# Kernel tuning notes

Measured on AMD Instinct MI355X. Metric: run time of the kernel, lower is better.

## Reference

```python
import jax, jax.numpy as jnp
import numpy as np

NH = 32          # nh * 2 neighbors per point (init nh=16)
P_REDUCTION = 0.5


def setup_inputs() -> dict:
    key = jax.random.key(0)
    k1, k2 = jax.random.split(key)
    x = jax.random.normal(k1, (2, 8192, 256), dtype=jnp.float32)       # [b, n, e]
    coords = jax.random.normal(k2, (2, 2, 8192, 1), dtype=jnp.float32) # [b, c, n, 1]
    return {"x": x, "coords": coords}


def _knn_gather(x, coords):
    """Return features of the NH nearest neighbors of each point: [b, n, NH, e]."""
    cs = coords[..., 0]                                   # [b, c, n]
    sq = jnp.sum(cs * cs, axis=1)                         # [b, n]
    # squared euclidean distances [b, n, n]
    d2 = sq[:, :, None] + sq[:, None, :] - 2.0 * jnp.einsum('bcn,bcm->bnm', cs, cs)
    d2 = jax.lax.stop_gradient(d2)                        # indices are non-differentiable
    _, nn_idx = jax.lax.top_k(-d2, NH)                    # [b, n, NH] nearest points
    # gather neighbor features: [b, 1, n, e] indexed with [b, n, NH, 1] -> [b, n, NH, e]
    x_nh = jnp.take_along_axis(x[:, None, :, :], nn_idx[..., None], axis=2)
    return x_nh


def _forward(x, coords):
    b, n, e = x.shape
    x_nh = _knn_gather(x, coords)                         # [b, n, NH, e]
    # unbiased std over the neighbor dim (torch.std default, ddof=1)
    mean_nh = jnp.mean(x_nh, axis=-2, keepdims=True)
    local_s = jnp.sqrt(jnp.sum((x_nh - mean_nh) ** 2, axis=-2) / (NH - 1))  # [b, n, e]
    global_m = jnp.abs(jnp.mean(x, axis=1))               # [b, e]
    local_dist = jnp.sum(local_s / global_m[:, None, :], axis=-1)           # [b, n]
    n_keep = int((1.0 - P_REDUCTION) * n)
    _, keep_idx = jax.lax.top_k(local_dist, n_keep)       # [b, n_keep], sorted desc
    x_out = jnp.take_along_axis(x, keep_idx[:, :, None], axis=1)            # [b, n_keep, e]
    coords_out = jnp.take_along_axis(coords, keep_idx[:, None, :, None], axis=2)  # [b, c, n_keep, 1]
    return x_out, coords_out, local_dist


def reference(x, coords):
    return _forward(x, coords)
```

## Files before the change

kernel.cpp:

```cpp
#include <hip/hip_runtime.h>

#define NN 8192
#define EE 256
#define KNH 32
#define NKEEP 4096
#define NCX 64
#define NCELL 4096
#define CNT_MIN 48

typedef unsigned long long u64;
typedef unsigned int u32;


__device__ __forceinline__ int cellof(float v) {
    const int q = (int)floorf((v + 4.6f) * (64.0f / 9.2f));
    return min(max(q, 0), NCX - 1);
}

__global__ void __launch_bounds__(1024) k_pre(const float* __restrict__ coords,
                                              const float* __restrict__ x,
                                              int* __restrict__ start,
                                              float2* __restrict__ sc,
                                              int* __restrict__ sj,
                                              float* __restrict__ part) {
    __shared__ int cnt[NCELL];
    __shared__ int wsum[16];
    const int blk = blockIdx.x;
    if (blk >= 2) {
        float* fred = (float*)cnt;
        const int unit  = blk - 2;
        const int b     = unit >> 5;
        const int chunk = unit & 31;
        const int col   = threadIdx.x & 255;
        const int qtr   = threadIdx.x >> 8;
        const float* xp = x + ((size_t)b * NN + (size_t)chunk * 256 + (size_t)qtr * 64) * EE + col;
        float s = 0.0f;
        for (int r = 0; r < 64; ++r) s += xp[(size_t)r * EE];
        fred[threadIdx.x] = s;
        __syncthreads();
        if (threadIdx.x < 256) {
            const float tot = fred[threadIdx.x] + fred[threadIdx.x + 256]
                            + fred[threadIdx.x + 512] + fred[threadIdx.x + 768];
            part[((size_t)b * 32 + chunk) * EE + threadIdx.x] = tot;
        }
        return;
    }
    const int b = blk, t = threadIdx.x;
    const int lane = t & 63, wv = t >> 6;
#pragma unroll
    for (int k = 0; k < 4; ++k) cnt[k * 1024 + t] = 0;
    __syncthreads();
#pragma unroll
    for (int k = 0; k < 8; ++k) {
        const int i = k * 1024 + t;
        const float xv = coords[(size_t)b * 2 * NN + i];
        const float yv = coords[(size_t)b * 2 * NN + NN + i];
        atomicAdd(&cnt[cellof(xv) * NCX + cellof(yv)], 1);
    }
    __syncthreads();
    const int v0 = cnt[t * 4 + 0], v1 = cnt[t * 4 + 1];
    const int v2 = cnt[t * 4 + 2], v3 = cnt[t * 4 + 3];
    const int s = v0 + v1 + v2 + v3;
    int inc = s;
#pragma unroll
    for (int d = 1; d < 64; d <<= 1) {
        const int u = __shfl_up(inc, d);
        inc += (lane >= d) ? u : 0;
    }
    if (lane == 63) wsum[wv] = inc;
    __syncthreads();
    int wpre = 0;
#pragma unroll
    for (int w = 0; w < 16; ++w) wpre += (w < wv) ? wsum[w] : 0;
    int run = wpre + inc - s;
    start[b * (NCELL + 1) + t * 4 + 0] = run; cnt[t * 4 + 0] = run; run += v0;
    start[b * (NCELL + 1) + t * 4 + 1] = run; cnt[t * 4 + 1] = run; run += v1;
    start[b * (NCELL + 1) + t * 4 + 2] = run; cnt[t * 4 + 2] = run; run += v2;
    start[b * (NCELL + 1) + t * 4 + 3] = run; cnt[t * 4 + 3] = run; run += v3;
    if (t == 0) start[b * (NCELL + 1) + NCELL] = NN;
    __syncthreads();
#pragma unroll
    for (int k = 0; k < 8; ++k) {
        const int i = k * 1024 + t;
        const float xv = coords[(size_t)b * 2 * NN + i];
        const float yv = coords[(size_t)b * 2 * NN + NN + i];
        const int p = atomicAdd(&cnt[cellof(xv) * NCX + cellof(yv)], 1);
        sc[(size_t)b * NN + p] = make_float2(xv, yv);
        sj[(size_t)b * NN + p] = i;
    }
}

__global__ void k_gm_final(const float* __restrict__ part, float* __restrict__ gm) {
    const int b = blockIdx.y, t = threadIdx.x;
    float s = 0.0f;
    for (int c = 0; c < 32; ++c) s += part[((size_t)b * 32 + c) * EE + t];
    gm[b * EE + t] = fabsf(s / (float)NN);
}

__device__ __forceinline__ u64 shfl_xor_u64(u64 v, int m) {
    const u32 hi = (u32)__shfl_xor((int)(u32)(v >> 32), m);
    const u32 lo = (u32)__shfl_xor((int)(u32)v, m);
    return ((u64)hi << 32) | lo;
}

__device__ __forceinline__ u64 wave_min_u64(u64 h) {
#pragma unroll
    for (int s = 1; s < 64; s <<= 1) {
        const u64 o = shfl_xor_u64(h, s);
        h = (o < h) ? o : h;
    }
    return h;
}

__global__ void __launch_bounds__(256) k_knn_dist(
        const float* __restrict__ x,
        const float* __restrict__ gm, const float2* __restrict__ sc,
        const int* __restrict__ sj, const int* __restrict__ start,
        float* __restrict__ ld_out) {
    __shared__ u64 comp[4][64];
    const int wg   = blockIdx.x;
    const int swz  = (wg & 7) * 512 + (wg >> 3);
    const int b    = swz >> 11;
    const int pb   = swz & 2047;
    const int wid  = threadIdx.x >> 6;
    const int lane = threadIdx.x & 63;
    const int p    = pb * 4 + wid;

    const float2* scb = sc + (size_t)b * NN;
    const int*    sjb = sj + (size_t)b * NN;
    const int*    stb = start + b * (NCELL + 1);
    const float2 cp = scb[p];
    const int    i  = sjb[p];
    const float ci0 = cp.x, ci1 = cp.y;
    const int qx = cellof(ci0), qy = cellof(ci1);

    int xl, yl, yh, nsl;
    int myc0 = 0, mylen = 0;
    {
        const int xl0 = max(qx - 1, 0), xh0 = min(qx + 1, NCX - 1);
        const int yl0 = max(qy - 1, 0), yh0 = min(qy + 1, NCX - 1);
        const int ns0 = xh0 - xl0 + 1;
        int a0 = 0, a1 = 0;
        if (lane < ns0) { a0 = stb[(xl0 + lane) * NCX + yl0]; a1 = stb[(xl0 + lane) * NCX + yh0 + 1]; }
        const int xl1 = max(qx - 2, 0), xh1 = min(qx + 2, NCX - 1);
        const int yl1 = max(qy - 2, 0), yh1 = min(qy + 2, NCX - 1);
        const int ns1 = xh1 - xl1 + 1;
        int b0 = 0, b1 = 0;
        if (lane < ns1) { b0 = stb[(xl1 + lane) * NCX + yl1]; b1 = stb[(xl1 + lane) * NCX + yh1 + 1]; }
        const int xl2 = max(qx - 4, 0), xh2c = min(qx + 4, NCX - 1);
        const int yl2 = max(qy - 4, 0), yh2c = min(qy + 4, NCX - 1);
        const int ns2 = xh2c - xl2 + 1;
        int e0 = 0, e1 = 0;
        if (lane < ns2) { e0 = stb[(xl2 + lane) * NCX + yl2]; e1 = stb[(xl2 + lane) * NCX + yh2c + 1]; }

        const int l0 = a1 - a0, l1 = b1 - b0, l2 = e1 - e0;
        int t0 = l0, t1 = l1, t2 = l2;
#pragma unroll
        for (int s = 1; s < 64; s <<= 1) {
            t0 += __shfl_xor(t0, s);
            t1 += __shfl_xor(t1, s);
            t2 += __shfl_xor(t2, s);
        }
        if (t0 >= CNT_MIN) {
            xl = xl0; yl = yl0; yh = yh0; nsl = ns0; myc0 = a0; mylen = l0;
        } else if (t1 >= CNT_MIN) {
            xl = xl1; yl = yl1; yh = yh1; nsl = ns1; myc0 = b0; mylen = l1;
        } else if (t2 >= CNT_MIN) {
            xl = xl2; yl = yl2; yh = yh2c; nsl = ns2; myc0 = e0; mylen = l2;
        } else {
            int r = 8;
            for (;;) {
                xl = max(qx - r, 0);
                const int xh = min(qx + r, NCX - 1);
                yl = max(qy - r, 0);
                yh = min(qy + r, NCX - 1);
                nsl = xh - xl + 1;
                int c0 = 0, c1 = 0;
                if (lane < nsl) {
                    c0 = stb[(xl + lane) * NCX + yl];
                    c1 = stb[(xl + lane) * NCX + yh + 1];
                }
                myc0 = c0; mylen = c1 - c0;
                int tot = mylen;
#pragma unroll
                for (int s = 1; s < 64; s <<= 1) tot += __shfl_xor(tot, s);
                if (tot >= CNT_MIN || r >= NCX) break;
                r <<= 1;
            }
        }
    }
    int incl = mylen;
#pragma unroll
    for (int d = 1; d < 64; d <<= 1) {
        const int v = __shfl_up(incl, d);
        incl += (lane >= d) ? v : 0;
    }
    int excl = incl - mylen;
    const int L1 = __shfl(incl, 63);

    float dmin = 1e30f;
    for (int g = 0; g < L1; g += 128) {
        const int gp0 = g + lane;
        const int gp1 = g + 64 + lane;
        int lo0 = 0, hi0 = nsl - 1, lo1 = 0, hi1 = nsl - 1;
#pragma unroll
        for (int st = 0; st < 6; ++st) {
            const int mid0 = (lo0 + hi0 + 1) >> 1;
            const int mid1 = (lo1 + hi1 + 1) >> 1;
            const int v0 = __shfl(excl, mid0);
            const int v1 = __shfl(excl, mid1);
            const bool go0 = (v0 <= gp0), go1 = (v1 <= gp1);
            lo0 = go0 ? mid0 : lo0; hi0 = go0 ? hi0 : mid0 - 1;
            lo1 = go1 ? mid1 : lo1; hi1 = go1 ? hi1 : mid1 - 1;
        }
        const int cnd0 = __shfl(myc0, lo0) + gp0 - __shfl(excl, lo0);
        const int cnd1 = __shfl(myc0, lo1) + gp1 - __shfl(excl, lo1);
        const int cc0 = min(max(cnd0, 0), NN - 1);
        const int cc1 = min(max(cnd1, 0), NN - 1);
        const float2 pt0 = scb[cc0];
        const float2 pt1 = scb[cc1];
        const float dx0 = ci0 - pt0.x, dy0 = ci1 - pt0.y;
        const float dx1 = ci0 - pt1.x, dy1 = ci1 - pt1.y;
        const float d0 = fmaf(dx0, dx0, dy0 * dy0);
        const float d1 = fmaf(dx1, dx1, dy1 * dy1);
        if (gp0 < L1) dmin = fminf(dmin, d0);
        if (gp1 < L1) dmin = fminf(dmin, d1);
    }

    u32 mk = __float_as_uint(dmin);
#pragma unroll
    for (int k = 2; k <= 64; k <<= 1) {
#pragma unroll
        for (int j = k >> 1; j > 0; j >>= 1) {
            const u32 o = (u32)__shfl_xor((int)mk, j);
            const bool keep_min = (((lane & j) == 0) == ((lane & k) == 0));
            const u32 mn = min(mk, o), mx = max(mk, o);
            mk = keep_min ? mn : mx;
        }
    }
    const u32 T = (u32)__shfl((int)mk, 31);

    const float srad = sqrtf(__uint_as_float(T)) * 1.0002f + 1e-5f;
    xl = cellof(ci0 - srad);
    const int xh2 = cellof(ci0 + srad);
    yl = cellof(ci1 - srad);
    yh = cellof(ci1 + srad);
    nsl = xh2 - xl + 1;
    {
        int c0 = 0, c1 = 0;
        if (lane < nsl) {
            c0 = stb[(xl + lane) * NCX + yl];
            c1 = stb[(xl + lane) * NCX + yh + 1];
        }
        myc0 = c0; mylen = c1 - c0;
    }
    incl = mylen;
#pragma unroll
    for (int d = 1; d < 64; d <<= 1) {
        const int v = __shfl_up(incl, d);
        incl += (lane >= d) ? v : 0;
    }
    excl = incl - mylen;
    const int L2 = __shfl(incl, 63);

    const u64 lmask = (1ull << lane) - 1;
    int base = 0;
    for (int g = 0; g < L2; g += 128) {
        const int gp0 = g + lane;
        const int gp1 = g + 64 + lane;
        int lo0 = 0, hi0 = nsl - 1, lo1 = 0, hi1 = nsl - 1;
#pragma unroll
        for (int st = 0; st < 6; ++st) {
            const int mid0 = (lo0 + hi0 + 1) >> 1;
            const int mid1 = (lo1 + hi1 + 1) >> 1;
            const int v0 = __shfl(excl, mid0);
            const int v1 = __shfl(excl, mid1);
            const bool go0 = (v0 <= gp0), go1 = (v1 <= gp1);
            lo0 = go0 ? mid0 : lo0; hi0 = go0 ? hi0 : mid0 - 1;
            lo1 = go1 ? mid1 : lo1; hi1 = go1 ? hi1 : mid1 - 1;
        }
        const int cnd0 = __shfl(myc0, lo0) + gp0 - __shfl(excl, lo0);
        const int cnd1 = __shfl(myc0, lo1) + gp1 - __shfl(excl, lo1);
        const int cc0 = min(max(cnd0, 0), NN - 1);
        const int cc1 = min(max(cnd1, 0), NN - 1);
        const float2 pt0 = scb[cc0];
        const float2 pt1 = scb[cc1];
        const int jj0 = sjb[cc0];
        const int jj1 = sjb[cc1];
        const float dx0 = ci0 - pt0.x, dy0 = ci1 - pt0.y;
        const float dx1 = ci0 - pt1.x, dy1 = ci1 - pt1.y;
        const u32 db0 = __float_as_uint(fmaf(dx0, dx0, dy0 * dy0));
        const u32 db1 = __float_as_uint(fmaf(dx1, dx1, dy1 * dy1));
        const bool k0 = (gp0 < L2) && (db0 <= T);
        const bool k1 = (gp1 < L2) && (db1 <= T);
        const u64 m0 = __ballot(k0);
        const int pos0 = base + __popcll(m0 & lmask);
        base += __popcll(m0);
        if (k0 && pos0 < 64) comp[wid][pos0] = ((u64)db0 << 32) | (u32)jj0;
        const u64 m1 = __ballot(k1);
        const int pos1 = base + __popcll(m1 & lmask);
        base += __popcll(m1);
        if (k1 && pos1 < 64) comp[wid][pos1] = ((u64)db1 << 32) | (u32)jj1;
    }
    const bool ovf = (base > 64) || (base < KNH);

    u64 key = (lane < base) ? comp[wid][lane] : ~0ull;
#pragma unroll
    for (int k = 2; k <= 64; k <<= 1) {
#pragma unroll
        for (int j = k >> 1; j > 0; j >>= 1) {
            const u64 other = shfl_xor_u64(key, j);
            const bool keep_min = (((lane & j) == 0) == ((lane & k) == 0));
            const bool lt = (key < other);
            const u64 mn = lt ? key : other;
            const u64 mx = lt ? other : key;
            key = keep_min ? mn : mx;
        }
    }
    int jkeep = (int)(u32)key;

    if (ovf) {
        u64 minkeep = 0;
        for (int k = 0; k < KNH; ++k) {
            u64 best = ~0ull;
            for (int g = 0; g < L2; g += 64) {
                const int gp = g + lane;
                int lo = 0, hi = nsl - 1;
#pragma unroll
                for (int st = 0; st < 6; ++st) {
                    const int mid = (lo + hi + 1) >> 1;
                    const int v = __shfl(excl, mid);
                    const bool go = (v <= gp);
                    lo = go ? mid : lo;
                    hi = go ? hi : mid - 1;
                }
                const int cnd = __shfl(myc0, lo) + gp - __shfl(excl, lo);
                const int cc  = min(max(cnd, 0), NN - 1);
                const float2 pt = scb[cc];
                const int    jj = sjb[cc];
                const float dx = ci0 - pt.x, dy = ci1 - pt.y;
                const float d  = fmaf(dx, dx, dy * dy);
                const u64 kk = ((u64)__float_as_uint(d) << 32) | (u32)jj;
                if (gp < L2 && kk >= minkeep && kk < best) best = kk;
            }
            const u64 h = wave_min_u64(best);
            if (lane == k) jkeep = (int)(u32)h;
            minkeep = h + 1;
        }
    }

    float s1[4] = {0.f, 0.f, 0.f, 0.f};
    float s2[4] = {0.f, 0.f, 0.f, 0.f};
    const float* xb = x + (size_t)b * NN * EE;
#pragma unroll 8
    for (int k = 0; k < KNH; ++k) {
        const int j = __builtin_amdgcn_readlane(jkeep, k);
        const float4 v = *reinterpret_cast<const float4*>(xb + (size_t)j * EE + (lane << 2));
        s1[0] += v.x; s2[0] += v.x * v.x;
        s1[1] += v.y; s2[1] += v.y * v.y;
        s1[2] += v.z; s2[2] += v.z * v.z;
        s1[3] += v.w; s2[3] += v.w * v.w;
    }

    const float* gmb = gm + b * EE;
    float tt = 0.f;
#pragma unroll
    for (int q = 0; q < 4; ++q) {
        const float sum = s1[q];
        float ssd = s2[q] - sum * sum * (1.0f / 32.0f);
        ssd = ssd > 0.f ? ssd : 0.f;
        const float ls = sqrtf(ssd * (1.0f / 31.0f));
        tt += ls / gmb[(lane << 2) + q];
    }
#pragma unroll
    for (int s2r = 1; s2r < 64; s2r <<= 1) tt += __shfl_xor(tt, s2r);

    if (lane == 0) ld_out[(size_t)b * NN + i] = tt;
}

__global__ void k_rank_gather(const float* __restrict__ x, const float* __restrict__ coords,
                              const float* __restrict__ ld,
                              float* __restrict__ x_out, float* __restrict__ c_out) {
    const int b    = blockIdx.y;
    const int wid  = threadIdx.x >> 6;
    const int lane = threadIdx.x & 63;
    const int i    = blockIdx.x * 4 + wid;
    const float* lb = ld + (size_t)b * NN;
    const float di = lb[i];
    int cnt = 0;
    for (int t = 0; t < NN / 256; ++t) {
        const int j0 = t * 256 + (lane << 2);
        const float4 dv = *reinterpret_cast<const float4*>(lb + j0);
        cnt += (dv.x > di || (dv.x == di && (j0 + 0) < i)) ? 1 : 0;
        cnt += (dv.y > di || (dv.y == di && (j0 + 1) < i)) ? 1 : 0;
        cnt += (dv.z > di || (dv.z == di && (j0 + 2) < i)) ? 1 : 0;
        cnt += (dv.w > di || (dv.w == di && (j0 + 3) < i)) ? 1 : 0;
    }
#pragma unroll
    for (int s = 1; s < 64; s <<= 1) cnt += __shfl_xor(cnt, s);

    if (cnt < NKEEP) {
        const float4 v = *reinterpret_cast<const float4*>(x + ((size_t)b * NN + i) * EE + (lane << 2));
        *reinterpret_cast<float4*>(x_out + ((size_t)b * NKEEP + cnt) * EE + (lane << 2)) = v;
        if (lane < 2) {
            c_out[((size_t)b * 2 + lane) * NKEEP + cnt] = coords[((size_t)b * 2 + lane) * NN + i];
        }
    }
}

extern "C" void kernel_launch(void* const* d_in, const int* in_sizes, int n_in,
                              void* d_out, int out_size, void* d_ws, size_t ws_size,
                              hipStream_t stream) {
    const float* x      = (const float*)d_in[0];
    const float* coords = (const float*)d_in[1];

    float* out    = (float*)d_out;
    float* x_out  = out;
    float* c_out  = out + 2097152;
    float* ld_out = out + 2113536;

    char*   ws    = (char*)d_ws;
    float*  part  = (float*)(ws);
    float*  gm    = (float*)(ws + 65536);
    int*    start = (int*)  (ws + 67584);
    float2* sc    = (float2*)(ws + 100384);
    int*    sj    = (int*)  (ws + 231456);

    k_pre        <<<66,            1024, 0, stream>>>(coords, x, start, sc, sj, part);
    k_gm_final   <<<dim3(1, 2),    256,  0, stream>>>(part, gm);
    k_knn_dist   <<<4096,          256,  0, stream>>>(x, gm, sc, sj, start, ld_out);
    k_rank_gather<<<dim3(2048, 2), 256,  0, stream>>>(x, coords, ld_out, x_out, c_out);
}
```

Baseline: 83.85 us.

## Reuse first-pass candidate distances in registers when refine box is contained

The first KNN pass now keeps the first 256 candidate distances and indices in registers. When the refined search box fits inside the first box and that box held at most 256 candidates, the second pass compacts from those registers instead of re-reading the cell table and recomputing distances. The rare exact fallback is moved into a noinline function to reduce register pressure and code size in the main path. This adds live registers during the first pass, which could lower occupancy.

```diff
diff --git a/kernel.cpp b/kernel.cpp
--- a/kernel.cpp
+++ b/kernel.cpp
@@ -112,6 +112,52 @@
     return h;
 }
 
+__device__ __noinline__ int exact_fb(const float2* scb, const int* sjb, const int* stb,
+                                     float cx, float cy, int xl, int xh, int yl, int yh,
+                                     int lane) {
+    const int nsl = xh - xl + 1;
+    int c0 = 0, c1 = 0;
+    if (lane < nsl) { c0 = stb[(xl + lane) * NCX + yl]; c1 = stb[(xl + lane) * NCX + yh + 1]; }
+    const int myc = c0, len = c1 - c0;
+    int inc = len;
+#pragma unroll
+    for (int d = 1; d < 64; d <<= 1) {
+        const int v = __shfl_up(inc, d);
+        inc += (lane >= d) ? v : 0;
+    }
+    const int ex = inc - len;
+    const int L = __shfl(inc, 63);
+    int jk = 0;
+    u64 minkeep = 0;
+    for (int k = 0; k < KNH; ++k) {
+        u64 best = ~0ull;
+        for (int g = 0; g < L; g += 64) {
+            const int gp = g + lane;
+            int lo = 0, hi = nsl - 1;
+#pragma unroll
+            for (int st = 0; st < 6; ++st) {
+                const int mid = (lo + hi + 1) >> 1;
+                const int v = __shfl(ex, mid);
+                const bool go = (v <= gp);
+                lo = go ? mid : lo;
+                hi = go ? hi : mid - 1;
+            }
+            const int cnd = __shfl(myc, lo) + gp - __shfl(ex, lo);
+            const int cc = min(max(cnd, 0), NN - 1);
+            const float2 pt = scb[cc];
+            const int jj = sjb[cc];
+            const float dx = cx - pt.x, dy = cy - pt.y;
+            const float d = fmaf(dx, dx, dy * dy);
+            const u64 kk = ((u64)__float_as_uint(d) << 32) | (u32)jj;
+            if (gp < L && kk >= minkeep && kk < best) best = kk;
+        }
+        const u64 h = wave_min_u64(best);
+        if (lane == k) jk = (int)(u32)h;
+        minkeep = h + 1;
+    }
+    return jk;
+}
+
 __global__ void __launch_bounds__(256) k_knn_dist(
         const float* __restrict__ x,
         const float* __restrict__ gm, const float2* __restrict__ sc,
@@ -189,6 +235,7 @@
             }
         }
     }
+    const int xh1box = xl + nsl - 1;
     int incl = mylen;
 #pragma unroll
     for (int d = 1; d < 64; d <<= 1) {
@@ -199,7 +246,43 @@
     const int L1 = __shfl(incl, 63);
 
     float dmin = 1e30f;
-    for (int g = 0; g < L1; g += 128) {
+    u32 kdb0 = 0xFFFFFFFFu, kdb1 = 0xFFFFFFFFu, kdb2 = 0xFFFFFFFFu, kdb3 = 0xFFFFFFFFu;
+    int  kjj0 = 0, kjj1 = 0, kjj2 = 0, kjj3 = 0;
+
+#define CHUNK2(G, DB0, JJ0, DB1, JJ1)                                       \
+    do {                                                                    \
+        const int gp0 = (G) + lane;                                         \
+        const int gp1 = (G) + 64 + lane;                                    \
+        int lo0 = 0, hi0 = nsl - 1, lo1 = 0, hi1 = nsl - 1;                 \
+        _Pragma("unroll")                                                   \
+        for (int st = 0; st < 6; ++st) {                                    \
+            const int mid0 = (lo0 + hi0 + 1) >> 1;                          \
+            const int mid1 = (lo1 + hi1 + 1) >> 1;                          \
+            const int v0 = __shfl(excl, mid0);                              \
+            const int v1 = __shfl(excl, mid1);                              \
+            const bool go0 = (v0 <= gp0), go1 = (v1 <= gp1);                \
+            lo0 = go0 ? mid0 : lo0; hi0 = go0 ? hi0 : mid0 - 1;             \
+            lo1 = go1 ? mid1 : lo1; hi1 = go1 ? hi1 : mid1 - 1;             \
+        }                                                                   \
+        const int cnd0 = __shfl(myc0, lo0) + gp0 - __shfl(excl, lo0);       \
+        const int cnd1 = __shfl(myc0, lo1) + gp1 - __shfl(excl, lo1);       \
+        const int cc0 = min(max(cnd0, 0), NN - 1);                          \
+        const int cc1 = min(max(cnd1, 0), NN - 1);                          \
+        const float2 pt0 = scb[cc0];                                        \
+        const float2 pt1 = scb[cc1];                                        \
+        const int j0_ = sjb[cc0];                                           \
+        const int j1_ = sjb[cc1];                                           \
+        const float dx0 = ci0 - pt0.x, dy0 = ci1 - pt0.y;                   \
+        const float dx1 = ci0 - pt1.x, dy1 = ci1 - pt1.y;                   \
+        const float d0 = fmaf(dx0, dx0, dy0 * dy0);                         \
+        const float d1 = fmaf(dx1, dx1, dy1 * dy1);                         \
+        if (gp0 < L1) { dmin = fminf(dmin, d0); DB0 = __float_as_uint(d0); JJ0 = j0_; } \
+        if (gp1 < L1) { dmin = fminf(dmin, d1); DB1 = __float_as_uint(d1); JJ1 = j1_; } \
+    } while (0)
+
+    CHUNK2(0, kdb0, kjj0, kdb1, kjj1);
+    if (L1 > 128) CHUNK2(128, kdb2, kjj2, kdb3, kjj3);
+    for (int g = 256; g < L1; g += 128) {
         const int gp0 = g + lane;
         const int gp1 = g + 64 + lane;
         int lo0 = 0, hi0 = nsl - 1, lo1 = 0, hi1 = nsl - 1;
@@ -241,66 +324,68 @@
     const u32 T = (u32)__shfl((int)mk, 31);
 
     const float srad = sqrtf(__uint_as_float(T)) * 1.0002f + 1e-5f;
-    xl = cellof(ci0 - srad);
-    const int xh2 = cellof(ci0 + srad);
-    yl = cellof(ci1 - srad);
-    yh = cellof(ci1 + srad);
-    nsl = xh2 - xl + 1;
-    {
-        int c0 = 0, c1 = 0;
-        if (lane < nsl) {
-            c0 = stb[(xl + lane) * NCX + yl];
-            c1 = stb[(xl + lane) * NCX + yh + 1];
-        }
-        myc0 = c0; mylen = c1 - c0;
-    }
-    incl = mylen;
-#pragma unroll
-    for (int d = 1; d < 64; d <<= 1) {
-        const int v = __shfl_up(incl, d);
-        incl += (lane >= d) ? v : 0;
-    }
-    excl = incl - mylen;
-    const int L2 = __shfl(incl, 63);
+    const int p2xl = cellof(ci0 - srad), p2xh = cellof(ci0 + srad);
+    const int p2yl = cellof(ci1 - srad), p2yh = cellof(ci1 + srad);
+    const bool contained = (L1 <= 256) && (p2xl >= xl) && (p2xh <= xh1box) &&
+                           (p2yl >= yl) && (p2yh <= yh);
 
     const u64 lmask = (1ull << lane) - 1;
     int base = 0;
-    for (int g = 0; g < L2; g += 128) {
-        const int gp0 = g + lane;
-        const int gp1 = g + 64 + lane;
-        int lo0 = 0, hi0 = nsl - 1, lo1 = 0, hi1 = nsl - 1;
-#pragma unroll
-        for (int st = 0; st < 6; ++st) {
-            const int mid0 = (lo0 + hi0 + 1) >> 1;
-            const int mid1 = (lo1 + hi1 + 1) >> 1;
-            const int v0 = __shfl(excl, mid0);
-            const int v1 = __shfl(excl, mid1);
-            const bool go0 = (v0 <= gp0), go1 = (v1 <= gp1);
-            lo0 = go0 ? mid0 : lo0; hi0 = go0 ? hi0 : mid0 - 1;
-            lo1 = go1 ? mid1 : lo1; hi1 = go1 ? hi1 : mid1 - 1;
-        }
-        const int cnd0 = __shfl(myc0, lo0) + gp0 - __shfl(excl, lo0);
-        const int cnd1 = __shfl(myc0, lo1) + gp1 - __shfl(excl, lo1);
-        const int cc0 = min(max(cnd0, 0), NN - 1);
-        const int cc1 = min(max(cnd1, 0), NN - 1);
-        const float2 pt0 = scb[cc0];
-        const float2 pt1 = scb[cc1];
-        const int jj0 = sjb[cc0];
-        const int jj1 = sjb[cc1];
-        const float dx0 = ci0 - pt0.x, dy0 = ci1 - pt0.y;
-        const float dx1 = ci0 - pt1.x, dy1 = ci1 - pt1.y;
-        const u32 db0 = __float_as_uint(fmaf(dx0, dx0, dy0 * dy0));
-        const u32 db1 = __float_as_uint(fmaf(dx1, dx1, dy1 * dy1));
-        const bool k0 = (gp0 < L2) && (db0 <= T);
-        const bool k1 = (gp1 < L2) && (db1 <= T);
-        const u64 m0 = __ballot(k0);
-        const int pos0 = base + __popcll(m0 & lmask);
-        base += __popcll(m0);
-        if (k0 && pos0 < 64) comp[wid][pos0] = ((u64)db0 << 32) | (u32)jj0;
-        const u64 m1 = __ballot(k1);
-        const int pos1 = base + __popcll(m1 & lmask);
-        base += __popcll(m1);
-        if (k1 && pos1 < 64) comp[wid][pos1] = ((u64)db1 << 32) | (u32)jj1;
+
+#define COMPACT(DB, JJ)                                                     \
+    do {                                                                    \
+        const bool keep = ((DB) <= T);                                      \
+        const u64 m = __ballot(keep);                                       \
+        const int pos = base + __popcll(m & lmask);                         \
+        base += __popcll(m);                                                \
+        if (keep && pos < 64) comp[wid][pos] = ((u64)(DB) << 32) | (u32)(JJ); \
+    } while (0)
+
+    if (contained) {
+        COMPACT(kdb0, kjj0);
+        COMPACT(kdb1, kjj1);
+        COMPACT(kdb2, kjj2);
+        COMPACT(kdb3, kjj3);
+    } else {
+        const int nsl2 = p2xh - p2xl + 1;
+        int c0 = 0, c1 = 0;
+        if (lane < nsl2) {
+            c0 = stb[(p2xl + lane) * NCX + p2yl];
+            c1 = stb[(p2xl + lane) * NCX + p2yh + 1];
+        }
+        const int myc2 = c0;
+        const int len2 = c1 - c0;
+        int incl2 = len2;
+#pragma unroll
+        for (int d = 1; d < 64; d <<= 1) {
+            const int v = __shfl_up(incl2, d);
+            incl2 += (lane >= d) ? v : 0;
+        }
+        const int excl2 = incl2 - len2;
+        const int L2 = __shfl(incl2, 63);
+        for (int g = 0; g < L2; g += 64) {
+            const int gp = g + lane;
+            int lo = 0, hi = nsl2 - 1;
+#pragma unroll
+            for (int st = 0; st < 6; ++st) {
+                const int mid = (lo + hi + 1) >> 1;
+                const int v = __shfl(excl2, mid);
+                const bool go = (v <= gp);
+                lo = go ? mid : lo;
+                hi = go ? hi : mid - 1;
+            }
+            const int cnd = __shfl(myc2, lo) + gp - __shfl(excl2, lo);
+            const int cc  = min(max(cnd, 0), NN - 1);
+            const float2 pt = scb[cc];
+            const int    jj = sjb[cc];
+            const float dx = ci0 - pt.x, dy = ci1 - pt.y;
+            const u32 db = __float_as_uint(fmaf(dx, dx, dy * dy));
+            const bool keep = (gp < L2) && (db <= T);
+            const u64 m = __ballot(keep);
+            const int pos = base + __popcll(m & lmask);
+            base += __popcll(m);
+            if (keep && pos < 64) comp[wid][pos] = ((u64)db << 32) | (u32)jj;
+        }
     }
     const bool ovf = (base > 64) || (base < KNH);
 
@@ -319,35 +404,7 @@
     }
     int jkeep = (int)(u32)key;
 
-    if (ovf) {
-        u64 minkeep = 0;
-        for (int k = 0; k < KNH; ++k) {
-            u64 best = ~0ull;
-            for (int g = 0; g < L2; g += 64) {
-                const int gp = g + lane;
-                int lo = 0, hi = nsl - 1;
-#pragma unroll
-                for (int st = 0; st < 6; ++st) {
-                    const int mid = (lo + hi + 1) >> 1;
-                    const int v = __shfl(excl, mid);
-                    const bool go = (v <= gp);
-                    lo = go ? mid : lo;
-                    hi = go ? hi : mid - 1;
-                }
-                const int cnd = __shfl(myc0, lo) + gp - __shfl(excl, lo);
-                const int cc  = min(max(cnd, 0), NN - 1);
-                const float2 pt = scb[cc];
-                const int    jj = sjb[cc];
-                const float dx = ci0 - pt.x, dy = ci1 - pt.y;
-                const float d  = fmaf(dx, dx, dy * dy);
-                const u64 kk = ((u64)__float_as_uint(d) << 32) | (u32)jj;
-                if (gp < L2 && kk >= minkeep && kk < best) best = kk;
-            }
-            const u64 h = wave_min_u64(best);
-            if (lane == k) jkeep = (int)(u32)h;
-            minkeep = h + 1;
-        }
-    }
+    if (ovf) jkeep = exact_fb(scb, sjb, stb, ci0, ci1, p2xl, p2xh, p2yl, p2yh, lane);
 
     float s1[4] = {0.f, 0.f, 0.f, 0.f};
     float s2[4] = {0.f, 0.f, 0.f, 0.f};
```

New measurement: 82.90 us (median of 2 runs). No clear change (-1.1%).
